# Kernel optimization log

Hardware: AMD Instinct MI355X
Metric: run time of the kernel (lower is better)

## Reference

```python
import jax, jax.numpy as jnp
import numpy as np

H_DIM, N_HEAD, FF_DIM, B_GRAPHS, MAX_N = 256, 8, 1024, 16, 512
LENGTHS = np.array([512, 480, 448, 416, 384, 352, 320, 288] * 2)  # ragged graph sizes, sum = 6400
N_NODES = int(LENGTHS.sum())
N_EDGES = 16 * N_NODES  # avg degree 16


def setup_inputs() -> dict:
    key = jax.random.key(0)
    kq, kk, kv, ko, k1, k2, kh = jax.random.split(key, 7)
    offsets = np.concatenate([[0], np.cumsum(LENGTHS)[:-1]])
    batch_np = np.repeat(np.arange(B_GRAPHS), LENGTHS)
    rng = np.random.default_rng(0)
    src = rng.integers(0, N_NODES, N_EDGES)
    g = batch_np[src]
    dst = offsets[g] + rng.integers(0, LENGTHS[g])  # dst in same graph as src
    edge_index = jnp.asarray(np.stack([src, dst]), dtype=jnp.int32)
    batch = jnp.asarray(batch_np, dtype=jnp.int32)

    def w(k, shape):
        return 0.02 * jax.random.normal(k, shape, dtype=jnp.float32)

    return dict(
        h=jax.random.normal(kh, (N_NODES, H_DIM), dtype=jnp.float32),
        Wq=w(kq, (H_DIM, H_DIM)), bq=jnp.zeros(H_DIM),
        Wk=w(kk, (H_DIM, H_DIM)), bk=jnp.zeros(H_DIM),
        Wv=w(kv, (H_DIM, H_DIM)), bv=jnp.zeros(H_DIM),
        Wo=w(ko, (H_DIM, H_DIM)), bo=jnp.zeros(H_DIM),
        W1=w(k1, (FF_DIM, H_DIM)), b1=jnp.zeros(FF_DIM),
        W2=w(k2, (H_DIM, FF_DIM)), b2=jnp.zeros(H_DIM),
        g1=jnp.ones(H_DIM), be1=jnp.zeros(H_DIM),
        g2=jnp.ones(H_DIM), be2=jnp.zeros(H_DIM),
        batch=batch, edge_index=edge_index,
        num_graphs=B_GRAPHS, max_n=MAX_N, n_head=N_HEAD,
    )


def _layernorm(x, g, b, eps=1e-5):
    mu = x.mean(-1, keepdims=True)
    var = ((x - mu) ** 2).mean(-1, keepdims=True)
    return (x - mu) * jax.lax.rsqrt(var + eps) * g + b


def reference(h, Wq, bq, Wk, bk, Wv, bv, Wo, bo, W1, b1, W2, b2, g1, be1, g2, be2,
              batch, edge_index, num_graphs, max_n, n_head):
    N, H = h.shape
    dh = H // n_head
    # position of each node inside its graph (batch is sorted by graph)
    counts = jax.ops.segment_sum(jnp.ones(N, jnp.int32), batch, num_segments=num_graphs)
    offsets = jnp.concatenate([jnp.zeros(1, jnp.int32), jnp.cumsum(counts)[:-1].astype(jnp.int32)])
    pos = jnp.arange(N, dtype=jnp.int32) - offsets[batch]
    # to_dense_batch: pad ragged nodes into [B, S, H]
    x = jnp.zeros((num_graphs, max_n, H), h.dtype).at[batch, pos].set(h)
    # to_dense_adj + _canonical_mask: faithful to source, EDGES get -inf (True -> -inf)
    src, dst = edge_index[0], edge_index[1]
    adj = jnp.zeros((num_graphs, max_n, max_n), bool).at[batch[src], pos[src], pos[dst]].set(True)
    attn_mask = jnp.where(adj, -jnp.inf, 0.0)[:, None, :, :]  # [B,1,S,S], broadcast over heads

    def proj(W, b):
        return (x @ W.T + b).reshape(num_graphs, max_n, n_head, dh).transpose(0, 2, 1, 3)

    q = proj(Wq, bq)
    k = proj(Wk, bk)
    v = proj(Wk, bk)  # faithful to source: V_x uses self.K
    scores = jax.nn.softmax(attn_mask + jnp.einsum('bhsd,bhtd->bhst', q, k) / np.sqrt(dh).astype(h.dtype), axis=-1)
    att = jnp.einsum('bhst,bhtd->bhsd', scores, v).transpose(0, 2, 1, 3).reshape(num_graphs, max_n, H)
    att = att @ Wo.T + bo
    h_att = att[batch, pos]  # from_dense_batch: unpad back to [N, H]
    h1 = _layernorm(h_att + h, g1, be1)
    ff = jax.nn.relu(h1 @ W1.T + b1) @ W2.T + b2
    return _layernorm(ff + h1, g2, be2)
```

## Files before the change

kernel.cpp:

```cpp
#include <hip/hip_runtime.h>
#include <math.h>

typedef unsigned int u32;
typedef unsigned short ushort_t;
typedef __attribute__((ext_vector_type(8))) short short8;
typedef __attribute__((ext_vector_type(4))) float f32x4;
typedef __attribute__((ext_vector_type(16))) float f32x16;

#define B_G 16
#define S_MAX 512
#define NH 8
#define DH 32
#define HD 256
#define FFD 1024
#define ADJW 16

__device__ __forceinline__ ushort_t f2bf(float f) {
  u32 u = __float_as_uint(f);
  u += 0x7fffu + ((u >> 16) & 1u);
  return (ushort_t)(u >> 16);
}
__device__ __forceinline__ float bf2f(ushort_t s) {
  return __uint_as_float(((u32)s) << 16);
}

__device__ __forceinline__ void gll16(const void* g, void* l) {
  __builtin_amdgcn_global_load_lds(
      (const __attribute__((address_space(1))) unsigned int*)g,
      (__attribute__((address_space(3))) unsigned int*)l, 16, 0, 0);
}

__global__ __launch_bounds__(256) void k_prep2(u32* __restrict__ adj,
    const int* __restrict__ batch, int N, int* __restrict__ offs,
    const float* __restrict__ bq, const float* __restrict__ bk, float* __restrict__ bqk,
    const float* __restrict__ wa, const float* __restrict__ wb, const float* __restrict__ wc,
    const float* __restrict__ wd, const float* __restrict__ we,
    ushort_t* __restrict__ oa, ushort_t* __restrict__ ob, ushort_t* __restrict__ oc,
    ushort_t* __restrict__ od, ushort_t* __restrict__ oe,
    const float* __restrict__ h, ushort_t* __restrict__ hb) {
  int blk = blockIdx.x, tid = threadIdx.x;
  if (blk < 128) {
    uint4 z = {0u, 0u, 0u, 0u};
    ((uint4*)adj)[blk * 256 + tid] = z;
  } else if (blk == 128) {
    bqk[tid] = bq[tid];
    bqk[HD + tid] = bk[tid];
    if (tid <= B_G) {
      if (tid == B_G) { offs[B_G] = N; }
      else {
        int lo = 0, hi = N;
        while (lo < hi) { int mid = (lo + hi) >> 1; if (batch[mid] < tid) lo = mid + 1; else hi = mid; }
        offs[tid] = lo;
      }
    }
  } else if (blk < 481) {
    int bb = blk - 129;
    const float* src; ushort_t* dst; int off;
    if (bb < 32)       { src = wa; dst = oa; off = bb; }
    else if (bb < 64)  { src = wb; dst = ob; off = bb - 32; }
    else if (bb < 96)  { src = wc; dst = oc; off = bb - 64; }
    else if (bb < 224) { src = wd; dst = od; off = bb - 96; }
    else               { src = we; dst = oe; off = bb - 224; }
    size_t i = (size_t)off * 2048 + tid * 8;
    float4 v0 = *(const float4*)&src[i];
    float4 v1 = *(const float4*)&src[i + 4];
    uint4 pk;
    pk.x = (u32)f2bf(v0.x) | ((u32)f2bf(v0.y) << 16);
    pk.y = (u32)f2bf(v0.z) | ((u32)f2bf(v0.w) << 16);
    pk.z = (u32)f2bf(v1.x) | ((u32)f2bf(v1.y) << 16);
    pk.w = (u32)f2bf(v1.z) | ((u32)f2bf(v1.w) << 16);
    *(uint4*)&dst[i] = pk;
  } else {
    size_t i = ((size_t)(blk - 481) * 256 + tid) * 8;
    float4 v0 = *(const float4*)&h[i];
    float4 v1 = *(const float4*)&h[i + 4];
    uint4 pk;
    pk.x = (u32)f2bf(v0.x) | ((u32)f2bf(v0.y) << 16);
    pk.y = (u32)f2bf(v0.z) | ((u32)f2bf(v0.w) << 16);
    pk.z = (u32)f2bf(v1.x) | ((u32)f2bf(v1.y) << 16);
    pk.w = (u32)f2bf(v1.z) | ((u32)f2bf(v1.w) << 16);
    *(uint4*)&hb[i] = pk;
  }
}

template<bool RELU, bool DOEDGE>
__global__ __launch_bounds__(256) void k_mgemm(const ushort_t* __restrict__ A,
    const ushort_t* __restrict__ W, const float* __restrict__ bias,
    ushort_t* __restrict__ Cout, int Ncols, int Kdim, int gridx,
    const int* __restrict__ ei, int E, const int* __restrict__ batch,
    const int* __restrict__ offs, u32* __restrict__ adj) {
  __shared__ __align__(16) ushort_t As[2][64 * 64];
  __shared__ __align__(16) ushort_t Bs[2][128 * 64];
  int tid = threadIdx.x;
  int wid = tid >> 6, lane = tid & 63;
  int wm = wid & 1, wn = wid >> 1;
  int arow0 = blockIdx.x * 64, bcol0 = blockIdx.y * 128;

  if (DOEDGE) {
    int e = (blockIdx.y * gridx + blockIdx.x) * 256 + tid;
    if (e < E) {
      int s = ei[e], d = ei[E + e];
      int b = batch[s];
      int o = offs[b];
      atomicOr(&adj[(b * S_MAX + (s - o)) * ADJW + ((d - o) >> 5)], 1u << ((d - o) & 31));
    }
  }

  const ushort_t* gA[2]; const ushort_t* gB[4];
  int dofsA[2], dofsB[4];
  #pragma unroll
  for (int i = 0; i < 2; i++) {
    int s = i * 256 + wid * 64 + lane;
    int r = s >> 3, ck = (s & 7) ^ (r & 7);
    gA[i] = A + (size_t)(arow0 + r) * Kdim + ck * 8;
    dofsA[i] = (i * 256 + wid * 64) * 8;
  }
  #pragma unroll
  for (int i = 0; i < 4; i++) {
    int s = i * 256 + wid * 64 + lane;
    int r = s >> 3, ck = (s & 7) ^ (r & 7);
    gB[i] = W + (size_t)(bcol0 + r) * Kdim + ck * 8;
    dofsB[i] = (i * 256 + wid * 64) * 8;
  }

  f32x4 acc[2][4];
  #pragma unroll
  for (int i = 0; i < 2; i++)
    #pragma unroll
    for (int j = 0; j < 4; j++) { f32x4 z = {0.f,0.f,0.f,0.f}; acc[i][j] = z; }

  #pragma unroll
  for (int i = 0; i < 2; i++) gll16(gA[i], &As[0][dofsA[i]]);
  #pragma unroll
  for (int i = 0; i < 4; i++) gll16(gB[i], &Bs[0][dofsB[i]]);
  asm volatile("s_waitcnt vmcnt(0)" ::: "memory");
  __builtin_amdgcn_s_barrier();

  int nsteps = Kdim >> 6;
  int cur = 0;
  for (int ks = 0; ks < nsteps; ks++) {
    if (ks + 1 < nsteps) {
      int k0n = (ks + 1) << 6;
      #pragma unroll
      for (int i = 0; i < 2; i++) gll16(gA[i] + k0n, &As[cur ^ 1][dofsA[i]]);
      #pragma unroll
      for (int i = 0; i < 4; i++) gll16(gB[i] + k0n, &Bs[cur ^ 1][dofsB[i]]);
    }
    #pragma unroll
    for (int kk = 0; kk < 2; kk++) {
      short8 af[2], bfv[4];
      #pragma unroll
      for (int i = 0; i < 2; i++) {
        int row = wm * 32 + i * 16 + (lane & 15);
        int ck = (kk * 4 + (lane >> 4)) ^ (row & 7);
        af[i] = *(const short8*)&As[cur][row * 64 + ck * 8];
      }
      #pragma unroll
      for (int j = 0; j < 4; j++) {
        int row = wn * 64 + j * 16 + (lane & 15);
        int ck = (kk * 4 + (lane >> 4)) ^ (row & 7);
        bfv[j] = *(const short8*)&Bs[cur][row * 64 + ck * 8];
      }
      #pragma unroll
      for (int i = 0; i < 2; i++)
        #pragma unroll
        for (int j = 0; j < 4; j++)
          acc[i][j] = __builtin_amdgcn_mfma_f32_16x16x32_bf16(af[i], bfv[j], acc[i][j], 0, 0, 0);
    }
    asm volatile("s_waitcnt vmcnt(0)" ::: "memory");
    __builtin_amdgcn_s_barrier();
    cur ^= 1;
  }

  float bj[4]; int colb[4];
  #pragma unroll
  for (int j = 0; j < 4; j++) {
    colb[j] = bcol0 + wn * 64 + j * 16 + (lane & 15);
    bj[j] = bias[colb[j]];
  }
  #pragma unroll
  for (int i = 0; i < 2; i++) {
    #pragma unroll
    for (int r = 0; r < 4; r++) {
      int row = arow0 + wm * 32 + i * 16 + (lane >> 4) * 4 + r;
      #pragma unroll
      for (int j = 0; j < 4; j++) {
        float v = acc[i][j][r] + bj[j];
        if (RELU) v = fmaxf(v, 0.f);
        Cout[(size_t)row * Ncols + colb[j]] = f2bf(v);
      }
    }
  }
}

template<bool OUTBF>
__global__ __launch_bounds__(256) void k_gemm_ln(const ushort_t* __restrict__ A,
    const ushort_t* __restrict__ W, const float* __restrict__ bias,
    const float* __restrict__ R, const float* __restrict__ gamma,
    const float* __restrict__ beta, float* __restrict__ outF,
    ushort_t* __restrict__ outB, int Kdim) {
  __shared__ __align__(16) ushort_t As[2][32 * 64];
  __shared__ __align__(16) ushort_t Bs[2][256 * 64];
  __shared__ float red_s[32 * 4];
  __shared__ float red_q[32 * 4];
  int tid = threadIdx.x;
  int wid = tid >> 6, lane = tid & 63;
  int wn = wid;
  int row0 = blockIdx.x * 32;

  const ushort_t* gA; int dofsA;
  {
    int r = tid >> 3, ck = (tid & 7) ^ (r & 7);
    gA = A + (size_t)(row0 + r) * Kdim + ck * 8;
    dofsA = (wid * 64) * 8;
  }
  const ushort_t* gB[8]; int dofsB[8];
  #pragma unroll
  for (int i = 0; i < 8; i++) {
    int s = i * 256 + tid;
    int r = s >> 3, ck = (s & 7) ^ (r & 7);
    gB[i] = W + (size_t)r * Kdim + ck * 8;
    dofsB[i] = (i * 256 + wid * 64) * 8;
  }

  f32x4 acc[2][4];
  #pragma unroll
  for (int i = 0; i < 2; i++)
    #pragma unroll
    for (int n = 0; n < 4; n++) { f32x4 z = {0.f,0.f,0.f,0.f}; acc[i][n] = z; }

  gll16(gA, &As[0][dofsA]);
  #pragma unroll
  for (int i = 0; i < 8; i++) gll16(gB[i], &Bs[0][dofsB[i]]);
  asm volatile("s_waitcnt vmcnt(0)" ::: "memory");
  __builtin_amdgcn_s_barrier();

  int nsteps = Kdim >> 6;
  int cur = 0;
  for (int ks = 0; ks < nsteps; ks++) {
    if (ks + 1 < nsteps) {
      int k0n = (ks + 1) << 6;
      gll16(gA + k0n, &As[cur ^ 1][dofsA]);
      #pragma unroll
      for (int i = 0; i < 8; i++) gll16(gB[i] + k0n, &Bs[cur ^ 1][dofsB[i]]);
    }
    #pragma unroll
    for (int kk = 0; kk < 2; kk++) {
      short8 af[2], bfv[4];
      #pragma unroll
      for (int i = 0; i < 2; i++) {
        int row = i * 16 + (lane & 15);
        int ck = (kk * 4 + (lane >> 4)) ^ (row & 7);
        af[i] = *(const short8*)&As[cur][row * 64 + ck * 8];
      }
      #pragma unroll
      for (int n = 0; n < 4; n++) {
        int row = wn * 64 + n * 16 + (lane & 15);
        int ck = (kk * 4 + (lane >> 4)) ^ (row & 7);
        bfv[n] = *(const short8*)&Bs[cur][row * 64 + ck * 8];
      }
      #pragma unroll
      for (int i = 0; i < 2; i++)
        #pragma unroll
        for (int n = 0; n < 4; n++)
          acc[i][n] = __builtin_amdgcn_mfma_f32_16x16x32_bf16(af[i], bfv[n], acc[i][n], 0, 0, 0);
    }
    asm volatile("s_waitcnt vmcnt(0)" ::: "memory");
    __builtin_amdgcn_s_barrier();
    cur ^= 1;
  }

  int col[4]; float bc[4], gm[4], bt[4];
  #pragma unroll
  for (int n = 0; n < 4; n++) {
    col[n] = wn * 64 + n * 16 + (lane & 15);
    bc[n] = bias[col[n]]; gm[n] = gamma[col[n]]; bt[n] = beta[col[n]];
  }
  #pragma unroll
  for (int i = 0; i < 2; i++) {
    #pragma unroll
    for (int r = 0; r < 4; r++) {
      int row_l = i * 16 + (lane >> 4) * 4 + r;
      const float* Rrow = R + (size_t)(row0 + row_l) * HD;
      float s = 0.f, q = 0.f;
      #pragma unroll
      for (int n = 0; n < 4; n++) {
        float v = acc[i][n][r] + bc[n] + Rrow[col[n]];
        acc[i][n][r] = v;
        s += v; q += v * v;
      }
      #pragma unroll
      for (int o = 1; o < 16; o <<= 1) { s += __shfl_xor(s, o, 64); q += __shfl_xor(q, o, 64); }
      if ((lane & 15) == 0) { red_s[row_l * 4 + wn] = s; red_q[row_l * 4 + wn] = q; }
    }
  }
  __syncthreads();
  #pragma unroll
  for (int i = 0; i < 2; i++) {
    #pragma unroll
    for (int r = 0; r < 4; r++) {
      int row_l = i * 16 + (lane >> 4) * 4 + r;
      float ssum = red_s[row_l * 4] + red_s[row_l * 4 + 1] + red_s[row_l * 4 + 2] + red_s[row_l * 4 + 3];
      float qsum = red_q[row_l * 4] + red_q[row_l * 4 + 1] + red_q[row_l * 4 + 2] + red_q[row_l * 4 + 3];
      float mu = ssum * (1.f / HD);
      float var = qsum * (1.f / HD) - mu * mu;
      float inv = rsqrtf(var + 1e-5f);
      size_t rb = (size_t)(row0 + row_l) * HD;
      #pragma unroll
      for (int n = 0; n < 4; n++) {
        float v = (acc[i][n][r] - mu) * inv * gm[n] + bt[n];
        outF[rb + col[n]] = v;
        if (OUTBF) outB[rb + col[n]] = f2bf(v);
      }
    }
  }
}

__global__ __launch_bounds__(256) void k_attn(const ushort_t* __restrict__ qkb,
    const u32* __restrict__ adj, const int* __restrict__ offs,
    const float* __restrict__ bqk, ushort_t* __restrict__ attOb) {
  int bid = blockIdx.x;
  int qtr = bid & 3, hh = (bid >> 2) & 7, b = bid >> 5;
  int nstart = offs[b], len = offs[b + 1] - nstart;
  int q0blk = qtr * 128;
  if (q0blk >= len) return;
  int lenT = len >> 5;

  __shared__ __align__(16) ushort_t K_lds[4 * 512 * 8];
  __shared__ __align__(16) ushort_t Kt_lds[64 * 32 * 8];
  __shared__ __align__(16) ushort_t P_lds[4 * 4 * 32 * 8];

  int tid = threadIdx.x;
  {
    const ushort_t* kg = qkb + (size_t)nstart * 512 + 256 + hh * 32;
    for (int t = tid; t < len; t += 256) {
      const uint4* src = (const uint4*)(kg + (size_t)t * 512);
      uint4 v0 = src[0], v1 = src[1], v2 = src[2], v3 = src[3];
      *(uint4*)&K_lds[0 * 4096 + t * 8] = v0;
      *(uint4*)&K_lds[1 * 4096 + t * 8] = v1;
      *(uint4*)&K_lds[2 * 4096 + t * 8] = v2;
      *(uint4*)&K_lds[3 * 4096 + t * 8] = v3;
    }
  }
  __syncthreads();
  {
    int d = tid & 31, tg = tid >> 5;
    int cc = d >> 3, e = d & 7;
    for (int i = 0; i < 8; i++) {
      int t0 = tg * 64 + i * 8;
      if (t0 < len) {
        u32 w0 = (u32)K_lds[cc * 4096 + (t0 + 0) * 8 + e] | ((u32)K_lds[cc * 4096 + (t0 + 1) * 8 + e] << 16);
        u32 w1 = (u32)K_lds[cc * 4096 + (t0 + 2) * 8 + e] | ((u32)K_lds[cc * 4096 + (t0 + 3) * 8 + e] << 16);
        u32 w2 = (u32)K_lds[cc * 4096 + (t0 + 4) * 8 + e] | ((u32)K_lds[cc * 4096 + (t0 + 5) * 8 + e] << 16);
        u32 w3 = (u32)K_lds[cc * 4096 + (t0 + 6) * 8 + e] | ((u32)K_lds[cc * 4096 + (t0 + 7) * 8 + e] << 16);
        uint4 pk = {w0, w1, w2, w3};
        *(uint4*)&Kt_lds[(t0 >> 3) * 256 + d * 8] = pk;
      }
    }
  }
  __syncthreads();

  int w = tid >> 6, lane = tid & 63;
  int q0w = q0blk + w * 32;
  if (q0w >= len) return;

  int lq = lane & 31, hf = lane >> 5;
  const float SCALE = 0.17677669529663687f;

  size_t qrow = (size_t)(nstart + q0w + lq) * 512 + hh * 32;
  short8 qf0 = *(const short8*)(qkb + qrow + hf * 8);
  short8 qf1 = *(const short8*)(qkb + qrow + 16 + hf * 8);

  const uint4* ap = (const uint4*)(adj + (size_t)(b * S_MAX + q0w + lq) * ADJW);
  uint4 a0 = ap[0], a1 = ap[1], a2 = ap[2], a3 = ap[3];
  u32 aw[16] = {a0.x, a0.y, a0.z, a0.w, a1.x, a1.y, a1.z, a1.w,
                a2.x, a2.y, a2.z, a2.w, a3.x, a3.y, a3.z, a3.w};

  f32x16 oacc = {0.f,0.f,0.f,0.f,0.f,0.f,0.f,0.f,0.f,0.f,0.f,0.f,0.f,0.f,0.f,0.f};
  float lsum = 0.f;

  for (int tt = 0; tt < lenT; tt++) {
    int t0 = tt * 32;
    short8 ka0 = *(const short8*)&K_lds[hf * 4096 + (t0 + lq) * 8];
    short8 ka1 = *(const short8*)&K_lds[(2 + hf) * 4096 + (t0 + lq) * 8];
    f32x16 sc = {0.f,0.f,0.f,0.f,0.f,0.f,0.f,0.f,0.f,0.f,0.f,0.f,0.f,0.f,0.f,0.f};
    sc = __builtin_amdgcn_mfma_f32_32x32x16_bf16(ka0, qf0, sc, 0, 0, 0);
    sc = __builtin_amdgcn_mfma_f32_32x32x16_bf16(ka1, qf1, sc, 0, 0, 0);
    u32 word = aw[tt];
    float p[16];
    #pragma unroll
    for (int r = 0; r < 16; r++) {
      int tb = (r & 3) + 8 * (r >> 2) + 4 * hf;
      float pe = __expf(sc[r] * SCALE);
      p[r] = ((word >> tb) & 1u) ? 0.f : pe;
      lsum += p[r];
    }
    #pragma unroll
    for (int g = 0; g < 4; g++) {
      u32 lo = (u32)f2bf(p[4 * g]) | ((u32)f2bf(p[4 * g + 1]) << 16);
      u32 hi = (u32)f2bf(p[4 * g + 2]) | ((u32)f2bf(p[4 * g + 3]) << 16);
      uint2 pk = {lo, hi};
      *(uint2*)&P_lds[w * 1024 + g * 256 + lq * 8 + hf * 4] = pk;
    }
    short8 va0 = *(const short8*)&Kt_lds[(t0 / 8 + hf) * 256 + lq * 8];
    short8 va1 = *(const short8*)&Kt_lds[(t0 / 8 + 2 + hf) * 256 + lq * 8];
    short8 pb0 = *(const short8*)&P_lds[w * 1024 + hf * 256 + lq * 8];
    short8 pb1 = *(const short8*)&P_lds[w * 1024 + (2 + hf) * 256 + lq * 8];
    oacc = __builtin_amdgcn_mfma_f32_32x32x16_bf16(va0, pb0, oacc, 0, 0, 0);
    oacc = __builtin_amdgcn_mfma_f32_32x32x16_bf16(va1, pb1, oacc, 0, 0, 0);
  }

  const float* bkh = bqk + 256 + hh * 32;
  float pq = 0.f;
  #pragma unroll
  for (int j = 0; j < 8; j++) pq += bf2f((ushort_t)qf0[j]) * bkh[hf * 8 + j];
  #pragma unroll
  for (int j = 0; j < 8; j++) pq += bf2f((ushort_t)qf1[j]) * bkh[16 + hf * 8 + j];
  pq += __shfl_xor(pq, 32, 64);
  float pe_pad = __expf(pq * SCALE) * (float)(S_MAX - len);

  float ltot = lsum + __shfl_xor(lsum, 32, 64) + pe_pad;
  float inv = 1.f / ltot;
  {
    int node = nstart + q0w + lq;
    ushort_t* op = attOb + (size_t)node * HD + hh * DH;
    #pragma unroll
    for (int g = 0; g < 4; g++) {
      float v0 = (oacc[4 * g]     + pe_pad * bkh[g * 8 + hf * 4 + 0]) * inv;
      float v1 = (oacc[4 * g + 1] + pe_pad * bkh[g * 8 + hf * 4 + 1]) * inv;
      float v2 = (oacc[4 * g + 2] + pe_pad * bkh[g * 8 + hf * 4 + 2]) * inv;
      float v3 = (oacc[4 * g + 3] + pe_pad * bkh[g * 8 + hf * 4 + 3]) * inv;
      u32 lo = (u32)f2bf(v0) | ((u32)f2bf(v1) << 16);
      u32 hi = (u32)f2bf(v2) | ((u32)f2bf(v3) << 16);
      uint2 pk = {lo, hi};
      *(uint2*)(op + g * 8 + hf * 4) = pk;
    }
  }
}

extern "C" void kernel_launch(void* const* d_in, const int* in_sizes, int n_in,
                              void* d_out, int out_size, void* d_ws, size_t ws_size,
                              hipStream_t stream) {
  const float* h   = (const float*)d_in[0];
  const float* Wq  = (const float*)d_in[1];
  const float* bq  = (const float*)d_in[2];
  const float* Wk  = (const float*)d_in[3];
  const float* bk  = (const float*)d_in[4];
  const float* Wo  = (const float*)d_in[7];
  const float* bo  = (const float*)d_in[8];
  const float* W1  = (const float*)d_in[9];
  const float* b1  = (const float*)d_in[10];
  const float* W2  = (const float*)d_in[11];
  const float* b2  = (const float*)d_in[12];
  const float* g1  = (const float*)d_in[13];
  const float* be1 = (const float*)d_in[14];
  const float* g2  = (const float*)d_in[15];
  const float* be2 = (const float*)d_in[16];
  const int* batch = (const int*)d_in[17];
  const int* ei    = (const int*)d_in[18];
  int N = in_sizes[0] / HD;
  int E = in_sizes[18] / 2;

  char* ws = (char*)d_ws;
  ushort_t* hb    = (ushort_t*)(ws);
  ushort_t* attOb = hb;
  ushort_t* qkb   = (ushort_t*)(ws + ((size_t)4 << 20));
  float*    h1    = (float*)(ws + ((size_t)12 << 20));
  ushort_t* h1b   = (ushort_t*)(ws + ((size_t)19 << 20));
  ushort_t* ff1b  = (ushort_t*)(ws + ((size_t)23 << 20));
  char* wbase = ws + ((size_t)36 << 20);
  ushort_t* Wqkb = (ushort_t*)(wbase);
  ushort_t* Wob  = (ushort_t*)(wbase + (256 << 10));
  ushort_t* W1b  = (ushort_t*)(wbase + (384 << 10));
  ushort_t* W2b  = (ushort_t*)(wbase + (896 << 10));
  float*    bqk  = (float*)(wbase + (1408 << 10));
  u32*      adj  = (u32*)(wbase + (1536 << 10));
  int*      offs = (int*)(ws + ((size_t)38 << 20));

  k_prep2<<<1281, 256, 0, stream>>>(adj, batch, N, offs, bq, bk, bqk,
                                    Wq, Wk, Wo, W1, W2,
                                    Wqkb, Wqkb + 65536, Wob, W1b, W2b, h, hb);
  k_mgemm<false, true><<<dim3(100, 4), 256, 0, stream>>>(hb, Wqkb, bqk, qkb, 512, HD, 100,
                                                         ei, E, batch, offs, adj);
  k_attn<<<B_G * NH * 4, 256, 0, stream>>>(qkb, adj, offs, bqk, attOb);
  k_gemm_ln<true><<<200, 256, 0, stream>>>(attOb, Wob, bo, h, g1, be1, h1, h1b, HD);
  k_mgemm<true, false><<<dim3(100, 8), 256, 0, stream>>>(h1b, W1b, b1, ff1b, FFD, HD, 100,
                                                         nullptr, 0, nullptr, nullptr, nullptr);
  k_gemm_ln<false><<<200, 256, 0, stream>>>(ff1b, W2b, b2, h1, g2, be2, (float*)d_out, nullptr, FFD);
}
```

Before: 88.07 us.

## Fuse output projection, LayerNorms and FFN into one tail kernel

Replaces the three post-attention launches (Wo GEMM+LN1, FFN1 GEMM with ReLU, FFN2 GEMM+LN2) with a single kernel. Each block of 32 rows keeps h1 and the FFN intermediate in LDS and registers and streams weight tiles through a triple-buffered pipeline. This removes the global round trips for h1, h1b and the 1024-wide ff1 activation and saves two launches. The trade-off is only 200 blocks, each reloading all weights, plus heavy LDS use that limits occupancy. The QK GEMM is also specialised with compile-time sizes.

```diff
diff --git a/kernel.cpp b/kernel.cpp
--- a/kernel.cpp
+++ b/kernel.cpp
@@ -83,10 +83,9 @@
   }
 }
 
-template<bool RELU, bool DOEDGE>
-__global__ __launch_bounds__(256) void k_mgemm(const ushort_t* __restrict__ A,
+__global__ __launch_bounds__(256) void k_qk(const ushort_t* __restrict__ A,
     const ushort_t* __restrict__ W, const float* __restrict__ bias,
-    ushort_t* __restrict__ Cout, int Ncols, int Kdim, int gridx,
+    ushort_t* __restrict__ Cout, int gridx,
     const int* __restrict__ ei, int E, const int* __restrict__ batch,
     const int* __restrict__ offs, u32* __restrict__ adj) {
   __shared__ __align__(16) ushort_t As[2][64 * 64];
@@ -96,7 +95,7 @@
   int wm = wid & 1, wn = wid >> 1;
   int arow0 = blockIdx.x * 64, bcol0 = blockIdx.y * 128;
 
-  if (DOEDGE) {
+  {
     int e = (blockIdx.y * gridx + blockIdx.x) * 256 + tid;
     if (e < E) {
       int s = ei[e], d = ei[E + e];
@@ -112,14 +111,14 @@
   for (int i = 0; i < 2; i++) {
     int s = i * 256 + wid * 64 + lane;
     int r = s >> 3, ck = (s & 7) ^ (r & 7);
-    gA[i] = A + (size_t)(arow0 + r) * Kdim + ck * 8;
+    gA[i] = A + (size_t)(arow0 + r) * HD + ck * 8;
     dofsA[i] = (i * 256 + wid * 64) * 8;
   }
   #pragma unroll
   for (int i = 0; i < 4; i++) {
     int s = i * 256 + wid * 64 + lane;
     int r = s >> 3, ck = (s & 7) ^ (r & 7);
-    gB[i] = W + (size_t)(bcol0 + r) * Kdim + ck * 8;
+    gB[i] = W + (size_t)(bcol0 + r) * HD + ck * 8;
     dofsB[i] = (i * 256 + wid * 64) * 8;
   }
 
@@ -136,10 +135,9 @@
   asm volatile("s_waitcnt vmcnt(0)" ::: "memory");
   __builtin_amdgcn_s_barrier();
 
-  int nsteps = Kdim >> 6;
   int cur = 0;
-  for (int ks = 0; ks < nsteps; ks++) {
-    if (ks + 1 < nsteps) {
+  for (int ks = 0; ks < 4; ks++) {
+    if (ks < 3) {
       int k0n = (ks + 1) << 6;
       #pragma unroll
       for (int i = 0; i < 2; i++) gll16(gA[i] + k0n, &As[cur ^ 1][dofsA[i]]);
@@ -184,134 +182,8 @@
     for (int r = 0; r < 4; r++) {
       int row = arow0 + wm * 32 + i * 16 + (lane >> 4) * 4 + r;
       #pragma unroll
-      for (int j = 0; j < 4; j++) {
-        float v = acc[i][j][r] + bj[j];
-        if (RELU) v = fmaxf(v, 0.f);
-        Cout[(size_t)row * Ncols + colb[j]] = f2bf(v);
-      }
-    }
-  }
-}
-
-template<bool OUTBF>
-__global__ __launch_bounds__(256) void k_gemm_ln(const ushort_t* __restrict__ A,
-    const ushort_t* __restrict__ W, const float* __restrict__ bias,
-    const float* __restrict__ R, const float* __restrict__ gamma,
-    const float* __restrict__ beta, float* __restrict__ outF,
-    ushort_t* __restrict__ outB, int Kdim) {
-  __shared__ __align__(16) ushort_t As[2][32 * 64];
-  __shared__ __align__(16) ushort_t Bs[2][256 * 64];
-  __shared__ float red_s[32 * 4];
-  __shared__ float red_q[32 * 4];
-  int tid = threadIdx.x;
-  int wid = tid >> 6, lane = tid & 63;
-  int wn = wid;
-  int row0 = blockIdx.x * 32;
-
-  const ushort_t* gA; int dofsA;
-  {
-    int r = tid >> 3, ck = (tid & 7) ^ (r & 7);
-    gA = A + (size_t)(row0 + r) * Kdim + ck * 8;
-    dofsA = (wid * 64) * 8;
-  }
-  const ushort_t* gB[8]; int dofsB[8];
-  #pragma unroll
-  for (int i = 0; i < 8; i++) {
-    int s = i * 256 + tid;
-    int r = s >> 3, ck = (s & 7) ^ (r & 7);
-    gB[i] = W + (size_t)r * Kdim + ck * 8;
-    dofsB[i] = (i * 256 + wid * 64) * 8;
-  }
-
-  f32x4 acc[2][4];
-  #pragma unroll
-  for (int i = 0; i < 2; i++)
-    #pragma unroll
-    for (int n = 0; n < 4; n++) { f32x4 z = {0.f,0.f,0.f,0.f}; acc[i][n] = z; }
-
-  gll16(gA, &As[0][dofsA]);
-  #pragma unroll
-  for (int i = 0; i < 8; i++) gll16(gB[i], &Bs[0][dofsB[i]]);
-  asm volatile("s_waitcnt vmcnt(0)" ::: "memory");
-  __builtin_amdgcn_s_barrier();
-
-  int nsteps = Kdim >> 6;
-  int cur = 0;
-  for (int ks = 0; ks < nsteps; ks++) {
-    if (ks + 1 < nsteps) {
-      int k0n = (ks + 1) << 6;
-      gll16(gA + k0n, &As[cur ^ 1][dofsA]);
-      #pragma unroll
-      for (int i = 0; i < 8; i++) gll16(gB[i] + k0n, &Bs[cur ^ 1][dofsB[i]]);
-    }
-    #pragma unroll
-    for (int kk = 0; kk < 2; kk++) {
-      short8 af[2], bfv[4];
-      #pragma unroll
-      for (int i = 0; i < 2; i++) {
-        int row = i * 16 + (lane & 15);
-        int ck = (kk * 4 + (lane >> 4)) ^ (row & 7);
-        af[i] = *(const short8*)&As[cur][row * 64 + ck * 8];
-      }
-      #pragma unroll
-      for (int n = 0; n < 4; n++) {
-        int row = wn * 64 + n * 16 + (lane & 15);
-        int ck = (kk * 4 + (lane >> 4)) ^ (row & 7);
-        bfv[n] = *(const short8*)&Bs[cur][row * 64 + ck * 8];
-      }
-      #pragma unroll
-      for (int i = 0; i < 2; i++)
-        #pragma unroll
-        for (int n = 0; n < 4; n++)
-          acc[i][n] = __builtin_amdgcn_mfma_f32_16x16x32_bf16(af[i], bfv[n], acc[i][n], 0, 0, 0);
-    }
-    asm volatile("s_waitcnt vmcnt(0)" ::: "memory");
-    __builtin_amdgcn_s_barrier();
-    cur ^= 1;
-  }
-
-  int col[4]; float bc[4], gm[4], bt[4];
-  #pragma unroll
-  for (int n = 0; n < 4; n++) {
-    col[n] = wn * 64 + n * 16 + (lane & 15);
-    bc[n] = bias[col[n]]; gm[n] = gamma[col[n]]; bt[n] = beta[col[n]];
-  }
-  #pragma unroll
-  for (int i = 0; i < 2; i++) {
-    #pragma unroll
-    for (int r = 0; r < 4; r++) {
-      int row_l = i * 16 + (lane >> 4) * 4 + r;
-      const float* Rrow = R + (size_t)(row0 + row_l) * HD;
-      float s = 0.f, q = 0.f;
-      #pragma unroll
-      for (int n = 0; n < 4; n++) {
-        float v = acc[i][n][r] + bc[n] + Rrow[col[n]];
-        acc[i][n][r] = v;
-        s += v; q += v * v;
-      }
-      #pragma unroll
-      for (int o = 1; o < 16; o <<= 1) { s += __shfl_xor(s, o, 64); q += __shfl_xor(q, o, 64); }
-      if ((lane & 15) == 0) { red_s[row_l * 4 + wn] = s; red_q[row_l * 4 + wn] = q; }
-    }
-  }
-  __syncthreads();
-  #pragma unroll
-  for (int i = 0; i < 2; i++) {
-    #pragma unroll
-    for (int r = 0; r < 4; r++) {
-      int row_l = i * 16 + (lane >> 4) * 4 + r;
-      float ssum = red_s[row_l * 4] + red_s[row_l * 4 + 1] + red_s[row_l * 4 + 2] + red_s[row_l * 4 + 3];
-      float qsum = red_q[row_l * 4] + red_q[row_l * 4 + 1] + red_q[row_l * 4 + 2] + red_q[row_l * 4 + 3];
-      float mu = ssum * (1.f / HD);
-      float var = qsum * (1.f / HD) - mu * mu;
-      float inv = rsqrtf(var + 1e-5f);
-      size_t rb = (size_t)(row0 + row_l) * HD;
-      #pragma unroll
-      for (int n = 0; n < 4; n++) {
-        float v = (acc[i][n][r] - mu) * inv * gm[n] + bt[n];
-        outF[rb + col[n]] = v;
-        if (OUTBF) outB[rb + col[n]] = f2bf(v);
-      }
+      for (int j = 0; j < 4; j++)
+        Cout[(size_t)row * 512 + colb[j]] = f2bf(acc[i][j][r] + bj[j]);
     }
   }
 }
@@ -436,6 +308,276 @@
       *(uint2*)(op + g * 8 + hf * 4) = pk;
     }
   }
+}
+
+__global__ __launch_bounds__(256) void k_tail(
+    const ushort_t* __restrict__ attOb, const ushort_t* __restrict__ Wob,
+    const float* __restrict__ bo, const float* __restrict__ hres,
+    const float* __restrict__ g1, const float* __restrict__ be1,
+    const ushort_t* __restrict__ W1b, const float* __restrict__ b1,
+    const ushort_t* __restrict__ W2b, const float* __restrict__ b2,
+    const float* __restrict__ g2, const float* __restrict__ be2,
+    float* __restrict__ outF) {
+  __shared__ __align__(16) ushort_t Ah[32 * 256];
+  __shared__ __align__(16) ushort_t Bst[3][16384];
+  __shared__ __align__(16) ushort_t Fc[32 * 128];
+  __shared__ __align__(16) float bv[2560];
+  __shared__ float red_s[128], red_q[128];
+  int tid = threadIdx.x, wid = tid >> 6, lane = tid & 63, wn = wid;
+  int row0 = blockIdx.x * 32;
+
+  #pragma unroll
+  for (int i = 0; i < 3; i++) {
+    int u = i * 256 + tid;
+    if (u < 640) {
+      int o = u * 4;
+      const float* src;
+      if      (o < 256)  src = bo  + o;
+      else if (o < 512)  src = g1  + (o - 256);
+      else if (o < 768)  src = be1 + (o - 512);
+      else if (o < 1024) src = b2  + (o - 768);
+      else if (o < 1280) src = g2  + (o - 1024);
+      else if (o < 1536) src = be2 + (o - 1280);
+      else               src = b1  + (o - 1536);
+      gll16(src, &bv[(i * 256 + wid * 64) * 4]);
+    }
+  }
+  float hr[2][4][4];
+  #pragma unroll
+  for (int m = 0; m < 2; m++)
+    #pragma unroll
+    for (int rr = 0; rr < 4; rr++) {
+      int row_l = m * 16 + (lane >> 4) * 4 + rr;
+      #pragma unroll
+      for (int n = 0; n < 4; n++)
+        hr[m][n][rr] = hres[(size_t)(row0 + row_l) * HD + wn * 64 + n * 16 + (lane & 15)];
+    }
+  #pragma unroll
+  for (int i = 0; i < 4; i++) {
+    int s = i * 256 + tid;
+    int r = s >> 5, ck = s & 31;
+    gll16(attOb + (size_t)(row0 + r) * HD + ((ck ^ (r & 7)) * 8),
+          &Ah[(i * 256 + wid * 64) * 8]);
+  }
+
+  auto STAGE = [&](int t, int buf) {
+    ushort_t* dst0 = &Bst[buf][0];
+    if (t < 4) {
+      #pragma unroll
+      for (int i = 0; i < 8; i++) {
+        int s = i * 256 + tid;
+        int r = s >> 3, ck = s & 7;
+        gll16(Wob + (size_t)r * HD + t * 64 + ((ck ^ (r & 7)) * 8),
+              dst0 + (i * 256 + wid * 64) * 8);
+      }
+    } else {
+      int u = t - 4, c = u >> 2, p = u & 3;
+      if (p < 2) {
+        #pragma unroll
+        for (int i = 0; i < 8; i++) {
+          int s = i * 256 + tid;
+          int r = s >> 4, ck = s & 15;
+          gll16(W1b + (size_t)(c * 128 + r) * HD + p * 128 + ((ck ^ (r & 7)) * 8),
+                dst0 + (i * 256 + wid * 64) * 8);
+        }
+      } else {
+        #pragma unroll
+        for (int i = 0; i < 8; i++) {
+          int s = i * 256 + tid;
+          int r = s >> 3, ck = s & 7;
+          gll16(W2b + (size_t)r * FFD + c * 128 + (p - 2) * 64 + ((ck ^ (r & 7)) * 8),
+                dst0 + (i * 256 + wid * 64) * 8);
+        }
+      }
+    }
+  };
+
+  f32x4 acc[2][4], ff2[2][4], acc1[2][2], hreg[2][4];
+  #pragma unroll
+  for (int m = 0; m < 2; m++)
+    #pragma unroll
+    for (int n = 0; n < 4; n++) { f32x4 z = {0.f,0.f,0.f,0.f}; acc[m][n] = z; ff2[m][n] = z; }
+
+  STAGE(0, 0); STAGE(1, 1); STAGE(2, 2);
+
+  for (int t = 0; t < 36; t++) {
+    if (t < 34) { asm volatile("s_waitcnt vmcnt(16)" ::: "memory"); }
+    else        { asm volatile("s_waitcnt vmcnt(0)" ::: "memory"); }
+    __builtin_amdgcn_s_barrier();
+    int buf = t % 3;
+    if (t < 4) {
+      #pragma unroll
+      for (int kk = 0; kk < 2; kk++) {
+        short8 af[2], bfv[4];
+        #pragma unroll
+        for (int m = 0; m < 2; m++) {
+          int r = m * 16 + (lane & 15);
+          int pos = (t * 8 + kk * 4 + (lane >> 4)) ^ (r & 7);
+          af[m] = *(const short8*)&Ah[r * 256 + pos * 8];
+        }
+        #pragma unroll
+        for (int n = 0; n < 4; n++) {
+          int rB = wn * 64 + n * 16 + (lane & 15);
+          int pos = (kk * 4 + (lane >> 4)) ^ (rB & 7);
+          bfv[n] = *(const short8*)&Bst[buf][rB * 64 + pos * 8];
+        }
+        #pragma unroll
+        for (int m = 0; m < 2; m++)
+          #pragma unroll
+          for (int n = 0; n < 4; n++)
+            acc[m][n] = __builtin_amdgcn_mfma_f32_16x16x32_bf16(af[m], bfv[n], acc[m][n], 0, 0, 0);
+      }
+    } else {
+      int u = t - 4, c = u >> 2, p = u & 3;
+      if (p < 2) {
+        if (p == 0) {
+          #pragma unroll
+          for (int m = 0; m < 2; m++)
+            #pragma unroll
+            for (int n = 0; n < 2; n++) { f32x4 z = {0.f,0.f,0.f,0.f}; acc1[m][n] = z; }
+        }
+        #pragma unroll
+        for (int kk = 0; kk < 4; kk++) {
+          short8 af[2], bfv[2];
+          #pragma unroll
+          for (int m = 0; m < 2; m++) {
+            int r = m * 16 + (lane & 15);
+            int pos = (p * 16 + kk * 4 + (lane >> 4)) ^ (r & 7);
+            af[m] = *(const short8*)&Ah[r * 256 + pos * 8];
+          }
+          #pragma unroll
+          for (int n = 0; n < 2; n++) {
+            int rB = wn * 32 + n * 16 + (lane & 15);
+            int pos = (kk * 4 + (lane >> 4)) ^ (rB & 7);
+            bfv[n] = *(const short8*)&Bst[buf][rB * 128 + pos * 8];
+          }
+          #pragma unroll
+          for (int m = 0; m < 2; m++)
+            #pragma unroll
+            for (int n = 0; n < 2; n++)
+              acc1[m][n] = __builtin_amdgcn_mfma_f32_16x16x32_bf16(af[m], bfv[n], acc1[m][n], 0, 0, 0);
+        }
+      } else {
+        #pragma unroll
+        for (int kk = 0; kk < 2; kk++) {
+          short8 af[2], bfv[4];
+          #pragma unroll
+          for (int m = 0; m < 2; m++) {
+            int r = m * 16 + (lane & 15);
+            int pos = ((p - 2) * 8 + kk * 4 + (lane >> 4)) ^ (r & 7);
+            af[m] = *(const short8*)&Fc[r * 128 + pos * 8];
+          }
+          #pragma unroll
+          for (int n = 0; n < 4; n++) {
+            int rB = wn * 64 + n * 16 + (lane & 15);
+            int pos = (kk * 4 + (lane >> 4)) ^ (rB & 7);
+            bfv[n] = *(const short8*)&Bst[buf][rB * 64 + pos * 8];
+          }
+          #pragma unroll
+          for (int m = 0; m < 2; m++)
+            #pragma unroll
+            for (int n = 0; n < 4; n++)
+              ff2[m][n] = __builtin_amdgcn_mfma_f32_16x16x32_bf16(af[m], bfv[n], ff2[m][n], 0, 0, 0);
+        }
+      }
+    }
+    if (t == 3) {
+      #pragma unroll
+      for (int m = 0; m < 2; m++)
+        #pragma unroll
+        for (int rr = 0; rr < 4; rr++) {
+          int row_l = m * 16 + (lane >> 4) * 4 + rr;
+          float s = 0.f, q = 0.f;
+          #pragma unroll
+          for (int n = 0; n < 4; n++) {
+            int col = wn * 64 + n * 16 + (lane & 15);
+            float v = acc[m][n][rr] + bv[col] + hr[m][n][rr];
+            acc[m][n][rr] = v;
+            s += v; q += v * v;
+          }
+          #pragma unroll
+          for (int o = 1; o < 16; o <<= 1) { s += __shfl_xor(s, o, 64); q += __shfl_xor(q, o, 64); }
+          if ((lane & 15) == 0) { red_s[row_l * 4 + wn] = s; red_q[row_l * 4 + wn] = q; }
+        }
+      asm volatile("s_waitcnt lgkmcnt(0)" ::: "memory");
+      __builtin_amdgcn_s_barrier();
+      #pragma unroll
+      for (int m = 0; m < 2; m++)
+        #pragma unroll
+        for (int rr = 0; rr < 4; rr++) {
+          int row_l = m * 16 + (lane >> 4) * 4 + rr;
+          float ssum = red_s[row_l * 4] + red_s[row_l * 4 + 1] + red_s[row_l * 4 + 2] + red_s[row_l * 4 + 3];
+          float qsum = red_q[row_l * 4] + red_q[row_l * 4 + 1] + red_q[row_l * 4 + 2] + red_q[row_l * 4 + 3];
+          float mu = ssum * (1.f / HD);
+          float var = qsum * (1.f / HD) - mu * mu;
+          float inv = rsqrtf(var + 1e-5f);
+          #pragma unroll
+          for (int n = 0; n < 4; n++) {
+            int col = wn * 64 + n * 16 + (lane & 15);
+            float v = (acc[m][n][rr] - mu) * inv * bv[256 + col] + bv[512 + col];
+            hreg[m][n][rr] = v;
+            int pos = ((col >> 3) ^ (row_l & 7));
+            Ah[row_l * 256 + pos * 8 + (col & 7)] = f2bf(v);
+          }
+        }
+      asm volatile("s_waitcnt lgkmcnt(0)" ::: "memory");
+    } else if (t >= 4 && ((t - 4) & 3) == 1) {
+      int c = (t - 4) >> 2;
+      #pragma unroll
+      for (int m = 0; m < 2; m++)
+        #pragma unroll
+        for (int rr = 0; rr < 4; rr++) {
+          int row_l = m * 16 + (lane >> 4) * 4 + rr;
+          #pragma unroll
+          for (int n = 0; n < 2; n++) {
+            int col = wn * 32 + n * 16 + (lane & 15);
+            float v = fmaxf(acc1[m][n][rr] + bv[1536 + c * 128 + col], 0.f);
+            int pos = ((col >> 3) ^ (row_l & 7));
+            Fc[row_l * 128 + pos * 8 + (col & 7)] = f2bf(v);
+          }
+        }
+      asm volatile("s_waitcnt lgkmcnt(0)" ::: "memory");
+    }
+    __builtin_amdgcn_s_barrier();
+    if (t + 3 < 36) STAGE(t + 3, (t + 3) % 3);
+  }
+
+  #pragma unroll
+  for (int m = 0; m < 2; m++)
+    #pragma unroll
+    for (int rr = 0; rr < 4; rr++) {
+      int row_l = m * 16 + (lane >> 4) * 4 + rr;
+      float s = 0.f, q = 0.f;
+      #pragma unroll
+      for (int n = 0; n < 4; n++) {
+        int col = wn * 64 + n * 16 + (lane & 15);
+        float v = ff2[m][n][rr] + bv[768 + col] + hreg[m][n][rr];
+        ff2[m][n][rr] = v;
+        s += v; q += v * v;
+      }
+      #pragma unroll
+      for (int o = 1; o < 16; o <<= 1) { s += __shfl_xor(s, o, 64); q += __shfl_xor(q, o, 64); }
+      if ((lane & 15) == 0) { red_s[row_l * 4 + wn] = s; red_q[row_l * 4 + wn] = q; }
+    }
+  asm volatile("s_waitcnt lgkmcnt(0)" ::: "memory");
+  __builtin_amdgcn_s_barrier();
+  #pragma unroll
+  for (int m = 0; m < 2; m++)
+    #pragma unroll
+    for (int rr = 0; rr < 4; rr++) {
+      int row_l = m * 16 + (lane >> 4) * 4 + rr;
+      float ssum = red_s[row_l * 4] + red_s[row_l * 4 + 1] + red_s[row_l * 4 + 2] + red_s[row_l * 4 + 3];
+      float qsum = red_q[row_l * 4] + red_q[row_l * 4 + 1] + red_q[row_l * 4 + 2] + red_q[row_l * 4 + 3];
+      float mu = ssum * (1.f / HD);
+      float var = qsum * (1.f / HD) - mu * mu;
+      float inv = rsqrtf(var + 1e-5f);
+      size_t rb = (size_t)(row0 + row_l) * HD;
+      #pragma unroll
+      for (int n = 0; n < 4; n++) {
+        int col = wn * 64 + n * 16 + (lane & 15);
+        outF[rb + col] = (ff2[m][n][rr] - mu) * inv * bv[1024 + col] + bv[1280 + col];
+      }
+    }
 }
 
 extern "C" void kernel_launch(void* const* d_in, const int* in_sizes, int n_in,
@@ -465,9 +607,6 @@
   ushort_t* hb    = (ushort_t*)(ws);
   ushort_t* attOb = hb;
   ushort_t* qkb   = (ushort_t*)(ws + ((size_t)4 << 20));
-  float*    h1    = (float*)(ws + ((size_t)12 << 20));
-  ushort_t* h1b   = (ushort_t*)(ws + ((size_t)19 << 20));
-  ushort_t* ff1b  = (ushort_t*)(ws + ((size_t)23 << 20));
   char* wbase = ws + ((size_t)36 << 20);
   ushort_t* Wqkb = (ushort_t*)(wbase);
   ushort_t* Wob  = (ushort_t*)(wbase + (256 << 10));
@@ -480,11 +619,9 @@
   k_prep2<<<1281, 256, 0, stream>>>(adj, batch, N, offs, bq, bk, bqk,
                                     Wq, Wk, Wo, W1, W2,
                                     Wqkb, Wqkb + 65536, Wob, W1b, W2b, h, hb);
-  k_mgemm<false, true><<<dim3(100, 4), 256, 0, stream>>>(hb, Wqkb, bqk, qkb, 512, HD, 100,
-                                                         ei, E, batch, offs, adj);
+  k_qk<<<dim3(100, 4), 256, 0, stream>>>(hb, Wqkb, bqk, qkb, 100,
+                                         ei, E, batch, offs, adj);
   k_attn<<<B_G * NH * 4, 256, 0, stream>>>(qkb, adj, offs, bqk, attOb);
-  k_gemm_ln<true><<<200, 256, 0, stream>>>(attOb, Wob, bo, h, g1, be1, h1, h1b, HD);
-  k_mgemm<true, false><<<dim3(100, 8), 256, 0, stream>>>(h1b, W1b, b1, ff1b, FFD, HD, 100,
-                                                         nullptr, 0, nullptr, nullptr, nullptr);
-  k_gemm_ln<false><<<200, 256, 0, stream>>>(ff1b, W2b, b2, h1, g2, be2, (float*)d_out, nullptr, FFD);
-}
+  k_tail<<<200, 256, 0, stream>>>(attOb, Wob, bo, h, g1, be1,
+                                  W1b, b1, W2b, b2, g2, be2, (float*)d_out);
+}
```

After: 94.99 us. 1.08x slower.
